# Kernel tuning notes

Measured on AMD Instinct MI355X. Metric: run time of the kernel, lower is better.

## Reference

```python
import jax, jax.numpy as jnp
import numpy as np

# HGT meta: 2 node types (A=0, B=1), 3 relations (src_type, dst_type)
L, T, R = 3, 2, 3
H, D = 1, 64            # PyG HGTConv default heads=1, head_dim = hidden/heads
F = H * D               # hidden_channels = input feature dim = 64
NA = NB = 131072
E = 1_000_000
REL = [(0, 1), (1, 0), (0, 0)]


def setup_inputs() -> dict:
    key = jax.random.key(0)
    ks = jax.random.split(key, 16)
    sc = 1.0 / np.sqrt(F)
    inp = {}
    inp["xA"] = jax.random.normal(ks[0], (NA, F), jnp.float32)
    inp["xB"] = jax.random.normal(ks[1], (NB, F), jnp.float32)
    # K/Q/V projections per (layer, node_type)
    inp["Wk"] = jax.random.normal(ks[2], (L, T, F, F), jnp.float32) * sc
    inp["bk"] = jnp.zeros((L, T, F), jnp.float32)
    inp["Wq"] = jax.random.normal(ks[3], (L, T, F, F), jnp.float32) * sc
    inp["bq"] = jnp.zeros((L, T, F), jnp.float32)
    inp["Wv"] = jax.random.normal(ks[4], (L, T, F, F), jnp.float32) * sc
    inp["bv"] = jnp.zeros((L, T, F), jnp.float32)
    # per (layer, relation, head) attention / message matrices and priority
    inp["a_rel"] = jax.random.normal(ks[5], (L, R, H, D, D), jnp.float32) * sc
    inp["m_rel"] = jax.random.normal(ks[6], (L, R, H, D, D), jnp.float32) * sc
    inp["p_rel"] = jnp.ones((L, R, H), jnp.float32)
    # output projection + skip gate per (layer, node_type)
    inp["Wa"] = jax.random.normal(ks[7], (L, T, F, F), jnp.float32) * sc
    inp["ba"] = jnp.zeros((L, T, F), jnp.float32)
    inp["skip"] = jnp.ones((L, T), jnp.float32)
    # final readout Linear(hidden, 1)
    inp["lin_w"] = jax.random.normal(ks[8], (F, 1), jnp.float32) * sc
    inp["lin_b"] = jnp.zeros((1,), jnp.float32)
    # edge indices: ei[0]=src, ei[1]=dst (NA == NB so one range works)
    inp["ei1"] = jax.random.randint(ks[9], (2, E), 0, NA, jnp.int32)   # A -> B
    inp["ei2"] = jax.random.randint(ks[10], (2, E), 0, NA, jnp.int32)  # B -> A
    inp["ei3"] = jax.random.randint(ks[11], (2, E), 0, NA, jnp.int32)  # A -> A
    return inp


def _hgt_layer(xs, eis, Wk, bk, Wq, bq, Wv, bv, a_rel, m_rel, p_rel, Wa, ba, skip):
    # per-type K/Q/V projections, reshaped to [N, H, D]
    k = [(xs[t] @ Wk[t] + bk[t]).reshape(-1, H, D) for t in range(T)]
    q = [(xs[t] @ Wq[t] + bq[t]).reshape(-1, H, D) for t in range(T)]
    v = [(xs[t] @ Wv[t] + bv[t]).reshape(-1, H, D) for t in range(T)]
    agg = [jnp.zeros((xs[t].shape[0], H, D), xs[t].dtype) for t in range(T)]
    inv_sqrt_d = jnp.asarray(1.0 / np.sqrt(D), xs[0].dtype)
    for r, (s, d) in enumerate(REL):
        src, dst = eis[r][0], eis[r][1]
        n_d = xs[d].shape[0]
        # relation-specific transforms on source nodes, then edge gather
        k_r = jnp.einsum('nhd,hde->nhe', k[s], a_rel[r])
        v_r = jnp.einsum('nhd,hde->nhe', v[s], m_rel[r])
        # attention score per edge per head: (q_dst . k_src) * p_rel / sqrt(D)
        score = jnp.einsum('ehd,ehd->eh', q[d][dst], k_r[src]) * p_rel[r] * inv_sqrt_d
        # segment softmax over incoming edges of each dst node (per edge type)
        mx = jax.ops.segment_max(score, dst, num_segments=n_d)
        ex = jnp.exp(score - mx[dst])
        den = jax.ops.segment_sum(ex, dst, num_segments=n_d)
        alpha = ex / den[dst]                      # [E, H]
        msg = alpha[:, :, None] * v_r[src]         # [E, H, D]
        agg[d] = agg[d] + jax.ops.segment_sum(msg, dst, num_segments=n_d)
    outs = []
    for t in range(T):
        o = jax.nn.gelu(agg[t].reshape(-1, F), approximate=False) @ Wa[t] + ba[t]
        a = jax.nn.sigmoid(skip[t])               # skip gate (out_dim == in_dim)
        outs.append(a * o + (1.0 - a) * xs[t])
    return outs


def reference(xA, xB, Wk, bk, Wq, bq, Wv, bv, a_rel, m_rel, p_rel, Wa, ba, skip,
              lin_w, lin_b, ei1, ei2, ei3):
    xs = [xA, xB]
    eis = [ei1, ei2, ei3]
    for l in range(L):
        xs = _hgt_layer(xs, eis, Wk[l], bk[l], Wq[l], bq[l], Wv[l], bv[l],
                        a_rel[l], m_rel[l], p_rel[l], Wa[l], ba[l], skip[l])
    x = jnp.concatenate(xs, axis=0)               # concat all node types
    pooled = jnp.sum(x, axis=0, keepdims=True)    # global_add_pool, batch=None
    return pooled @ lin_w + lin_b                 # Linear(hidden, 1) -> [1, 1]
```

## Files before the change

kernel.cpp:

```cpp
#include <hip/hip_runtime.h>
#include <cmath>

#define DEV __device__ __forceinline__

typedef __attribute__((ext_vector_type(8))) short short8v;
typedef __attribute__((ext_vector_type(4))) float f32x4;

DEV float atomicAddF(float* p, float v) {
    return unsafeAtomicAdd(p, v);
}

DEV float gelu_exact(float v) {
    return 0.5f * v * (1.f + erff(v * 0.70710678118654752f));
}

DEV unsigned short f32_to_bf16(float f) {
    union { float f; unsigned int u; } x; x.f = f;
    unsigned int r = x.u + 0x7fffu + ((x.u >> 16) & 1u);
    return (unsigned short)(r >> 16);
}

DEV unsigned int f4_to_fp8x4(float a, float b, float c, float d) {
    int r = __builtin_amdgcn_cvt_pk_fp8_f32(a, b, 0, false);
    r = __builtin_amdgcn_cvt_pk_fp8_f32(c, d, r, true);
    return (unsigned int)r;
}

DEV float4 fp8x4_to_f4(unsigned int w) {
    auto lo = __builtin_amdgcn_cvt_pk_f32_fp8(w, false);
    auto hi = __builtin_amdgcn_cvt_pk_f32_fp8(w, true);
    return make_float4(lo[0], lo[1], hi[0], hi[1]);
}

DEV short8v cvt8_bf16(float4 f0, float4 f1) {
    union { unsigned int u[4]; short8v s; } r;
    asm("v_cvt_pk_bf16_f32 %0, %1, %2" : "=v"(r.u[0]) : "v"(f0.x), "v"(f0.y));
    asm("v_cvt_pk_bf16_f32 %0, %1, %2" : "=v"(r.u[1]) : "v"(f0.z), "v"(f0.w));
    asm("v_cvt_pk_bf16_f32 %0, %1, %2" : "=v"(r.u[2]) : "v"(f1.x), "v"(f1.y));
    asm("v_cvt_pk_bf16_f32 %0, %1, %2" : "=v"(r.u[3]) : "v"(f1.z), "v"(f1.w));
    return r.s;
}


struct MatSetB {
    const unsigned short* Wt[3];
    const float* b[3];
    float*       y[3];
    int          mode[3];
    int          n;
};

#define BCAP2 6144
#define SB_TILE 4096
#define PSTR 129

__global__ __launch_bounds__(256) void combine_w_bf16(
    const float* __restrict__ Wk, const float* __restrict__ bk,
    const float* __restrict__ Wv, const float* __restrict__ bv,
    const float* __restrict__ a_rel, const float* __restrict__ m_rel,
    const float* __restrict__ p_rel, unsigned short* __restrict__ CWt,
    float* __restrict__ Cb)
{
    const int r = blockIdx.x, kv = blockIdx.y, l = blockIdx.z;
    const int srcT[3] = {0, 1, 0};
    const int s = srcT[r];
    const float* Wsrc = (kv == 0 ? Wk : Wv) + ((size_t)(l*2 + s)) * 4096;
    const float* bsrc = (kv == 0 ? bk : bv) + ((size_t)(l*2 + s)) * 64;
    const float* A    = (kv == 0 ? a_rel : m_rel) + ((size_t)(l*3 + r)) * 4096;
    const float scale = (kv == 0) ? p_rel[l*3 + r] * 0.125f : 1.f;

    __shared__ float Ws[4096];
    __shared__ float As[4096];
    const int tid = threadIdx.x;
    for (int k = tid; k < 4096; k += 256) { Ws[k] = Wsrc[k]; As[k] = A[k]; }
    __syncthreads();

    unsigned short* out = CWt + ((size_t)(l*6 + r*2 + kv)) * 4096;
    const int j = tid & 63;
    #pragma unroll
    for (int i = 0; i < 16; i++) {
        const int f = (tid >> 6) * 16 + i;
        float acc = 0.f;
        #pragma unroll
        for (int e = 0; e < 64; e++) acc = fmaf(Ws[f*64 + e], As[e*64 + j], acc);
        const int so = (l == 0) ? f : (4*(f & 15) + (f >> 4));
        out[j*64 + so] = f32_to_bf16(acc * scale);
    }
    if (tid < 64) {
        float acc = 0.f;
        for (int e = 0; e < 64; e++) acc = fmaf(bsrc[e], As[e*64 + tid], acc);
        Cb[(size_t)(l*6 + r*2 + kv) * 64 + tid] = acc * scale;
    }
}

__global__ __launch_bounds__(256) void prep_wt(
    const float* __restrict__ Wq, const float* __restrict__ Wa,
    unsigned short* __restrict__ Wqt, unsigned short* __restrict__ Wat)
{
    const int bid = blockIdx.x;
    const float* src; unsigned short* dst; int useSigma;
    if (bid < 6) { src = Wq + (size_t)bid * 4096; dst = Wqt + (size_t)bid * 4096;
                   useSigma = (bid >= 2); }
    else         { src = Wa + (size_t)(bid - 6) * 4096; dst = Wat + (size_t)(bid - 6) * 4096;
                   useSigma = 1; }
    for (int idx = threadIdx.x; idx < 4096; idx += 256) {
        const int c = idx >> 6, s = idx & 63;
        const int k = useSigma ? (16*(s & 3) + (s >> 2)) : s;
        dst[c*64 + s] = f32_to_bf16(src[k*64 + c]);
    }
}

__global__ __launch_bounds__(256) void proj_mfma(const float* __restrict__ x, MatSetB ms)
{
    const int tid = threadIdx.x;
    const int wv  = tid >> 6;
    const int ln  = tid & 63;
    const int j   = ln & 15;
    const int g   = ln >> 4;
    const long long rowb = (long long)blockIdx.x * 128 + wv * 32;

    short8v A[2][2];
    #pragma unroll
    for (int rg = 0; rg < 2; rg++) {
        const float* xp = x + (rowb + rg*16 + j) * 64 + g*8;
        #pragma unroll
        for (int ks = 0; ks < 2; ks++) {
            const float4 f0 = *(const float4*)(xp + ks*32);
            const float4 f1 = *(const float4*)(xp + ks*32 + 4);
            A[rg][ks] = cvt8_bf16(f0, f1);
        }
    }

    unsigned int kst[2][4];
    for (int m = 0; m < ms.n; m++) {
        short8v B[4][2];
        #pragma unroll
        for (int ct = 0; ct < 4; ct++) {
            const unsigned short* wp = ms.Wt[m] + (ct*16 + j) * 64 + g*8;
            B[ct][0] = *(const short8v*)(wp);
            B[ct][1] = *(const short8v*)(wp + 32);
        }
        f32x4 acc[2][4];
        #pragma unroll
        for (int ct = 0; ct < 4; ct++) {
            const float bm = ms.b[m][ct*16 + j];
            f32x4 bi = {bm, bm, bm, bm};
            acc[0][ct] = bi; acc[1][ct] = bi;
        }
        #pragma unroll
        for (int rg = 0; rg < 2; rg++)
            #pragma unroll
            for (int ct = 0; ct < 4; ct++) {
                acc[rg][ct] = __builtin_amdgcn_mfma_f32_16x16x32_bf16(
                    A[rg][0], B[ct][0], acc[rg][ct], 0, 0, 0);
                acc[rg][ct] = __builtin_amdgcn_mfma_f32_16x16x32_bf16(
                    A[rg][1], B[ct][1], acc[rg][ct], 0, 0, 0);
            }
        const int mode = ms.mode[m];
        if (mode == 0) {
            float* yb = ms.y[m];
            #pragma unroll
            for (int rg = 0; rg < 2; rg++)
                #pragma unroll
                for (int i = 0; i < 4; i++) {
                    const long long node = rowb + rg*16 + g*4 + i;
                    *(float4*)(yb + node*64 + j*4) = make_float4(
                        acc[rg][0][i], acc[rg][1][i], acc[rg][2][i], acc[rg][3][i]);
                }
        } else if (mode == 1) {
            #pragma unroll
            for (int rg = 0; rg < 2; rg++)
                #pragma unroll
                for (int i = 0; i < 4; i++)
                    kst[rg][i] = f4_to_fp8x4(
                        acc[rg][0][i], acc[rg][1][i], acc[rg][2][i], acc[rg][3][i]);
        } else {
            unsigned char* yb = (unsigned char*)ms.y[m];
            #pragma unroll
            for (int rg = 0; rg < 2; rg++)
                #pragma unroll
                for (int i = 0; i < 4; i++) {
                    const long long node = rowb + rg*16 + g*4 + i;
                    uint2 s;
                    s.x = kst[rg][i];
                    s.y = f4_to_fp8x4(
                        acc[rg][0][i], acc[rg][1][i], acc[rg][2][i], acc[rg][3][i]);
                    *(uint2*)(yb + node*128 + j*8) = s;
                }
        }
    }
}

__global__ __launch_bounds__(256) void scatter_bucket(
    const int* __restrict__ ei, int E, int nbuck,
    int* __restrict__ bcur, int2* __restrict__ pairbuf)
{
    __shared__ int  hist[256];
    __shared__ int  lbase[256];
    __shared__ int  gbase[256];
    __shared__ int  lcur[256];
    __shared__ int  scanbuf[256];
    __shared__ int2 stage[SB_TILE];
    const int tid = threadIdx.x;
    const int tile0 = blockIdx.x * SB_TILE;

    int2 my[16]; int mb[16];
    #pragma unroll
    for (int i = 0; i < 16; i++) {
        const int e = tile0 + tid + i*256;
        if (e < E) { my[i].x = ei[e]; my[i].y = ei[E + e]; mb[i] = my[i].y >> 9; }
        else mb[i] = -1;
    }
    hist[tid] = 0;
    __syncthreads();
    #pragma unroll
    for (int i = 0; i < 16; i++) if (mb[i] >= 0) atomicAdd(&hist[mb[i]], 1);
    __syncthreads();
    const int c = hist[tid];
    scanbuf[tid] = c;
    __syncthreads();
    for (int off = 1; off < 256; off <<= 1) {
        int add = (tid >= off) ? scanbuf[tid - off] : 0;
        __syncthreads();
        scanbuf[tid] += add;
        __syncthreads();
    }
    lbase[tid] = scanbuf[tid] - c;
    lcur[tid]  = scanbuf[tid] - c;
    if (c > 0 && tid < nbuck) gbase[tid] = atomicAdd(bcur + tid * 16, c);
    __syncthreads();
    #pragma unroll
    for (int i = 0; i < 16; i++) {
        if (mb[i] >= 0) {
            const int p = atomicAdd(&lcur[mb[i]], 1);
            stage[p] = my[i];
        }
    }
    __syncthreads();
    if (c > 0 && tid < nbuck) {
        const int gb = gbase[tid];
        const int lb = lbase[tid];
        int2* dstp = pairbuf + (size_t)tid * BCAP2;
        for (int jj = 0; jj < c; jj++) {
            const int gp = gb + jj;
            if (gp < BCAP2) dstp[gp] = stage[lb + jj];
        }
    }
}

__global__ __launch_bounds__(256) void bucket_csr(
    const int2* __restrict__ pairbuf, const int* __restrict__ bcur,
    int* __restrict__ row_ptr, int* __restrict__ row_end,
    int* __restrict__ col, int n)
{
    const int b   = blockIdx.x;
    const int tid = threadIdx.x;
    __shared__ int lcnt[512];
    __shared__ int lcur[512];
    __shared__ int scanbuf[256];
    int cnt = bcur[b * 16];
    if (cnt > BCAP2) cnt = BCAP2;
    lcnt[tid] = 0; lcnt[tid + 256] = 0;
    __syncthreads();
    const int2* src = pairbuf + (size_t)b * BCAP2;
    for (int i = tid; i < cnt; i += 256)
        atomicAdd(&lcnt[src[i].y & 511], 1);
    __syncthreads();
    const int c0 = lcnt[2*tid], c1 = lcnt[2*tid + 1];
    const int s = c0 + c1;
    scanbuf[tid] = s;
    __syncthreads();
    for (int off = 1; off < 256; off <<= 1) {
        int add = (tid >= off) ? scanbuf[tid - off] : 0;
        __syncthreads();
        scanbuf[tid] += add;
        __syncthreads();
    }
    const int excl = scanbuf[tid] - s;
    const int base = b * BCAP2;
    const int d0 = (b << 9) + 2*tid;
    if (d0 < n)     { row_ptr[d0]   = base + excl;      row_end[d0]   = base + excl + c0; }
    if (d0 + 1 < n) { row_ptr[d0+1] = base + excl + c0; row_end[d0+1] = base + excl + c0 + c1; }
    lcur[2*tid] = excl; lcur[2*tid + 1] = excl + c0;
    __syncthreads();
    for (int i = tid; i < cnt; i += 256) {
        const int2 p = src[i];
        const int pos = atomicAdd(&lcur[p.y & 511], 1);
        col[base + pos] = p.x;
    }
}

__global__ __launch_bounds__(128) void tile_perm(
    const int* __restrict__ rp1, const int* __restrict__ re1,
    const int* __restrict__ rp2, const int* __restrict__ re2,
    int dual, int n, unsigned char* __restrict__ perm)
{
    const int t   = threadIdx.x;
    const int dst = blockIdx.x * 128 + t;
    int deg = 0;
    if (dst < n) {
        deg = re1[dst] - rp1[dst];
        if (dual) deg += re2[dst] - rp2[dst];
    }
    __shared__ int degs[128];
    degs[t] = deg;
    __syncthreads();
    int rank = 0;
    for (int i = 0; i < 128; i++) {
        const int di = degs[i];
        rank += (di > deg) || (di == deg && i < t);
    }
    perm[(size_t)blockIdx.x * 128 + rank] = (unsigned char)t;
}

#define PROC_EDGE(KVR)                                                                 \
    {                                                                                  \
        const float4 ka_ = fp8x4_to_f4(KVR.x);                                         \
        const float4 kb2_ = fp8x4_to_f4(KVR.z);                                        \
        float sc_ = q0.x*ka_.x + q0.y*ka_.y + q0.z*ka_.z + q0.w*ka_.w                  \
                  + q1.x*kb2_.x + q1.y*kb2_.y + q1.z*kb2_.z + q1.w*kb2_.w;             \
        sc_ += __shfl_xor(sc_, 1); sc_ += __shfl_xor(sc_, 2); sc_ += __shfl_xor(sc_, 4);\
        const float p_ = __expf(sc_);                                                  \
        const float4 va_ = fp8x4_to_f4(KVR.y);                                         \
        const float4 vb_ = fp8x4_to_f4(KVR.w);                                         \
        ssum_ += p_;                                                                   \
        acc0_.x = fmaf(p_, va_.x, acc0_.x); acc0_.y = fmaf(p_, va_.y, acc0_.y);        \
        acc0_.z = fmaf(p_, va_.z, acc0_.z); acc0_.w = fmaf(p_, va_.w, acc0_.w);        \
        acc1_.x = fmaf(p_, vb_.x, acc1_.x); acc1_.y = fmaf(p_, vb_.y, acc1_.y);        \
        acc1_.z = fmaf(p_, vb_.z, acc1_.z); acc1_.w = fmaf(p_, vb_.w, acc1_.w);        \
    }

#define AGG_BODY(RP, RE, COL, KV, O0, O1)                                              \
    {                                                                                  \
        float4 acc0_ = {0.f,0.f,0.f,0.f}, acc1_ = {0.f,0.f,0.f,0.f};                   \
        float ssum_ = 0.f;                                                             \
        const int ss0_ = (RP)[dst], ss1_ = (RE)[dst];                                  \
        const unsigned char* kb_ = (KV) + sub*16;                                      \
        int e_ = ss0_;                                                                 \
        uint4 cc0_ = {0,0,0,0}, cc1_ = {0,0,0,0};                                      \
        if (e_ < ss1_)     cc0_ = *(const uint4*)(kb_ + (size_t)(COL)[e_] * 128);      \
        if (e_ + 1 < ss1_) cc1_ = *(const uint4*)(kb_ + (size_t)(COL)[e_+1] * 128);    \
        for (; e_ + 2 < ss1_; e_ += 2) {                                               \
            const int nn0_ = (COL)[e_+2];                                              \
            const int nn1_ = (e_ + 3 < ss1_) ? (COL)[e_+3] : nn0_;                     \
            const uint4 pp0_ = *(const uint4*)(kb_ + (size_t)nn0_ * 128);              \
            const uint4 pp1_ = *(const uint4*)(kb_ + (size_t)nn1_ * 128);              \
            PROC_EDGE(cc0_)                                                            \
            PROC_EDGE(cc1_)                                                            \
            cc0_ = pp0_; cc1_ = pp1_;                                                  \
        }                                                                              \
        if (e_ < ss1_)     PROC_EDGE(cc0_)                                             \
        if (e_ + 1 < ss1_) PROC_EDGE(cc1_)                                             \
        const float inv_ = (ssum_ > 0.f) ? 1.f / ssum_ : 0.f;                          \
        O0.x = fmaf(acc0_.x, inv_, O0.x); O0.y = fmaf(acc0_.y, inv_, O0.y);            \
        O0.z = fmaf(acc0_.z, inv_, O0.z); O0.w = fmaf(acc0_.w, inv_, O0.w);            \
        O1.x = fmaf(acc1_.x, inv_, O1.x); O1.y = fmaf(acc1_.y, inv_, O1.y);            \
        O1.z = fmaf(acc1_.z, inv_, O1.z); O1.w = fmaf(acc1_.w, inv_, O1.w);            \
    }

__global__ __launch_bounds__(1024, 8) void agg_epilogue(
    const int* __restrict__ rp1, const int* __restrict__ re1, const int* __restrict__ c1,
    const int* __restrict__ rp2, const int* __restrict__ re2, const int* __restrict__ c2,
    const float* __restrict__ q,
    const unsigned char* __restrict__ kva, const unsigned char* __restrict__ kvb,
    const unsigned char* __restrict__ perm,
    float* __restrict__ xio, const unsigned short* __restrict__ Wat,
    const float* __restrict__ ba, const float* __restrict__ skipw,
    int xstd, int dual, int dopool, float* __restrict__ vec)
{
    __shared__ float lds[64 * PSTR];
    __shared__ float lds_pool[64];
    const int tid = threadIdx.x;
    const long long rowb = (long long)blockIdx.x * 128;
    if (tid < 64) lds_pool[tid] = 0.f;

    {
        const int sub = tid & 7;
        const int dl  = perm[(size_t)blockIdx.x * 128 + (tid >> 3)];
        const int dst = (int)rowb + dl;
        const float4* qp = (const float4*)(q + (size_t)dst * 64);
        const float4 q0 = qp[sub*2], q1 = qp[sub*2 + 1];
        float4 o0 = {0.f,0.f,0.f,0.f}, o1 = {0.f,0.f,0.f,0.f};
        AGG_BODY(rp1, re1, c1, kva, o0, o1)
        if (dual) {
            AGG_BODY(rp2, re2, c2, kvb, o0, o1)
        }
        float* lp = lds + (size_t)(8*sub) * PSTR + dl;
        lp[0*PSTR] = gelu_exact(o0.x); lp[1*PSTR] = gelu_exact(o0.y);
        lp[2*PSTR] = gelu_exact(o0.z); lp[3*PSTR] = gelu_exact(o0.w);
        lp[4*PSTR] = gelu_exact(o1.x); lp[5*PSTR] = gelu_exact(o1.y);
        lp[6*PSTR] = gelu_exact(o1.z); lp[7*PSTR] = gelu_exact(o1.w);
    }
    __syncthreads();

    if (tid < 512) {
        const int wv = tid >> 6;
        const int ln = tid & 63;
        const int j  = ln & 15;
        const int g  = ln >> 4;
        const int r  = wv*16 + j;

        short8v A[2];
        #pragma unroll
        for (int ks = 0; ks < 2; ks++) {
            const int pb = g*8 + ks*32;
            const float4 f0 = make_float4(lds[(pb+0)*PSTR + r], lds[(pb+1)*PSTR + r],
                                          lds[(pb+2)*PSTR + r], lds[(pb+3)*PSTR + r]);
            const float4 f1 = make_float4(lds[(pb+4)*PSTR + r], lds[(pb+5)*PSTR + r],
                                          lds[(pb+6)*PSTR + r], lds[(pb+7)*PSTR + r]);
            A[ks] = cvt8_bf16(f0, f1);
        }

        f32x4 acc[4];
        #pragma unroll
        for (int ct = 0; ct < 4; ct++) {
            const float bm = ba[ct*16 + j];
            acc[ct] = (f32x4){bm, bm, bm, bm};
        }
        #pragma unroll
        for (int ct = 0; ct < 4; ct++) {
            const unsigned short* wp = Wat + (ct*16 + j) * 64 + g*8;
            const short8v B0 = *(const short8v*)(wp);
            const short8v B1 = *(const short8v*)(wp + 32);
            acc[ct] = __builtin_amdgcn_mfma_f32_16x16x32_bf16(A[0], B0, acc[ct], 0, 0, 0);
            acc[ct] = __builtin_amdgcn_mfma_f32_16x16x32_bf16(A[1], B1, acc[ct], 0, 0, 0);
        }

        const float gate = 1.f / (1.f + __expf(-skipw[0]));
        const float og   = 1.f - gate;
        float4 pacc = {0.f,0.f,0.f,0.f};
        #pragma unroll
        for (int i = 0; i < 4; i++) {
            const long long node = rowb + wv*16 + g*4 + i;
            float* xp = xio + node*64;
            float4 o;
            if (xstd) {
                o.x = gate*acc[0][i] + og*xp[j];
                o.y = gate*acc[1][i] + og*xp[16 + j];
                o.z = gate*acc[2][i] + og*xp[32 + j];
                o.w = gate*acc[3][i] + og*xp[48 + j];
            } else {
                const float4 xo = *(const float4*)(xp + 4*j);
                o = make_float4(gate*acc[0][i] + og*xo.x,
                                gate*acc[1][i] + og*xo.y,
                                gate*acc[2][i] + og*xo.z,
                                gate*acc[3][i] + og*xo.w);
            }
            if (!dopool) {
                *(float4*)(xp + 4*j) = o;
            } else {
                pacc.x += o.x; pacc.y += o.y; pacc.z += o.z; pacc.w += o.w;
            }
        }
        if (dopool) {
            atomicAdd(&lds_pool[4*j + 0], pacc.x);
            atomicAdd(&lds_pool[4*j + 1], pacc.y);
            atomicAdd(&lds_pool[4*j + 2], pacc.z);
            atomicAdd(&lds_pool[4*j + 3], pacc.w);
        }
    }
    __syncthreads();
    if (dopool && tid < 64) atomicAddF(vec + tid, lds_pool[tid]);
}

__global__ void final_dot(const float* __restrict__ vec, const float* __restrict__ lw,
                          const float* __restrict__ lb, float* __restrict__ out)
{
    const int i = threadIdx.x;
    float v = vec[i] * lw[16*(i & 3) + (i >> 2)];
    #pragma unroll
    for (int m = 32; m >= 1; m >>= 1) v += __shfl_xor(v, m);
    if (i == 0) out[0] = v + lb[0];
}

extern "C" void kernel_launch(void* const* d_in, const int* in_sizes, int n_in,
                              void* d_out, int out_size, void* d_ws, size_t ws_size,
                              hipStream_t stream)
{
    float* xs[2] = {(float*)d_in[0], (float*)d_in[1]};
    const float* Wk    = (const float*)d_in[2];
    const float* bk    = (const float*)d_in[3];
    const float* Wq    = (const float*)d_in[4];
    const float* bq    = (const float*)d_in[5];
    const float* Wv    = (const float*)d_in[6];
    const float* bv    = (const float*)d_in[7];
    const float* a_rel = (const float*)d_in[8];
    const float* m_rel = (const float*)d_in[9];
    const float* p_rel = (const float*)d_in[10];
    const float* Wa    = (const float*)d_in[11];
    const float* ba    = (const float*)d_in[12];
    const float* skipw = (const float*)d_in[13];
    const float* lin_w = (const float*)d_in[14];
    const float* lin_b = (const float*)d_in[15];
    const int*   ei[3] = {(const int*)d_in[16], (const int*)d_in[17], (const int*)d_in[18]};

    const long long NA = in_sizes[0] / 64;
    const long long NB = in_sizes[1] / 64;
    const long long Ns[2] = {NA, NB};
    const long long Nmax = NA > NB ? NA : NB;
    int E[3];
    for (int r = 0; r < 3; r++) E[r] = in_sizes[16 + r] / 2;
    static const int dstN_is_B[3] = {1, 0, 0};
    const long long nbuckMax = (Nmax + 511) >> 9;

    float* w = (float*)d_ws;
    float* qbuf  = w; w += Nmax * 64;
    unsigned char* kv0 = (unsigned char*)w; w += Nmax * 32;
    unsigned char* kv1 = (unsigned char*)w; w += Nmax * 32;
    unsigned short* CWt = (unsigned short*)w; w += 18 * 2048;
    unsigned short* Wqt = (unsigned short*)w; w += 6 * 2048;
    unsigned short* Wat = (unsigned short*)w; w += 6 * 2048;
    float* Cb    = w; w += 18 * 64;
    float* vec   = w; w += 64;
    unsigned char* permB = (unsigned char*)w; w += Nmax / 4;
    unsigned char* permA = (unsigned char*)w; w += Nmax / 4;
    int* iw = (int*)w;
    int* row_ptr[3]; int* row_end[3]; int* col[3];
    for (int r = 0; r < 3; r++) {
        row_ptr[r] = iw; iw += Nmax;
        row_end[r] = iw; iw += Nmax;
        col[r]     = iw; iw += nbuckMax * BCAP2;
    }
    int*  bcur    = iw; iw += nbuckMax * 16;
    int2* pairbuf = (int2*)iw;

    combine_w_bf16<<<dim3(3, 2, 3), 256, 0, stream>>>(Wk, bk, Wv, bv, a_rel, m_rel, p_rel, CWt, Cb);
    prep_wt<<<12, 256, 0, stream>>>(Wq, Wa, Wqt, Wat);
    hipMemsetAsync(vec, 0, 64 * sizeof(float), stream);

    for (int r = 0; r < 3; r++) {
        const int n = (int)Ns[dstN_is_B[r]];
        const int nbuck = (n + 511) >> 9;
        hipMemsetAsync(bcur, 0, (size_t)nbuck * 16 * sizeof(int), stream);
        scatter_bucket<<<(E[r] + SB_TILE - 1) / SB_TILE, 256, 0, stream>>>(
            ei[r], E[r], nbuck, bcur, pairbuf);
        bucket_csr<<<nbuck, 256, 0, stream>>>(pairbuf, bcur, row_ptr[r], row_end[r], col[r], n);
    }
    tile_perm<<<(int)((NB + 127) / 128), 128, 0, stream>>>(
        row_ptr[0], row_end[0], row_ptr[0], row_end[0], 0, (int)NB, permB);
    tile_perm<<<(int)((NA + 127) / 128), 128, 0, stream>>>(
        row_ptr[1], row_end[1], row_ptr[2], row_end[2], 1, (int)NA, permA);

    const int gA = (int)(NA >> 7), gB = (int)(NB >> 7);
    for (int l = 0; l < 3; l++) {
        const int xstd   = (l == 0) ? 1 : 0;
        const int dopool = (l == 2) ? 1 : 0;
        {
            MatSetB ms; ms.n = 3;
            ms.Wt[0] = Wqt + (size_t)(l*2 + 1) * 4096;  ms.b[0] = bq + (size_t)(l*2 + 1) * 64;
            ms.y[0] = qbuf;        ms.mode[0] = 0;
            ms.Wt[1] = CWt + (size_t)(l*6 + 2) * 4096;  ms.b[1] = Cb + (size_t)(l*6 + 2) * 64;
            ms.y[1] = nullptr;     ms.mode[1] = 1;
            ms.Wt[2] = CWt + (size_t)(l*6 + 3) * 4096;  ms.b[2] = Cb + (size_t)(l*6 + 3) * 64;
            ms.y[2] = (float*)kv1; ms.mode[2] = 2;
            proj_mfma<<<gB, 256, 0, stream>>>(xs[1], ms);
        }
        {
            MatSetB ms; ms.n = 2;
            ms.Wt[0] = CWt + (size_t)(l*6 + 0) * 4096;  ms.b[0] = Cb + (size_t)(l*6 + 0) * 64;
            ms.y[0] = nullptr;     ms.mode[0] = 1;
            ms.Wt[1] = CWt + (size_t)(l*6 + 1) * 4096;  ms.b[1] = Cb + (size_t)(l*6 + 1) * 64;
            ms.y[1] = (float*)kv0; ms.mode[1] = 2;
            ms.Wt[2] = ms.Wt[1]; ms.b[2] = ms.b[1]; ms.y[2] = ms.y[1]; ms.mode[2] = 2;
            proj_mfma<<<gA, 256, 0, stream>>>(xs[0], ms);
        }
        agg_epilogue<<<gB, 1024, 0, stream>>>(
            row_ptr[0], row_end[0], col[0],
            row_ptr[0], row_end[0], col[0],
            qbuf, kv0, kv0, permB, xs[1],
            Wat + (size_t)(l*2 + 1) * 4096, ba + (size_t)(l*2 + 1) * 64,
            skipw + l*2 + 1, xstd, 0, dopool, vec);

        {
            MatSetB ms; ms.n = 3;
            ms.Wt[0] = Wqt + (size_t)(l*2 + 0) * 4096;  ms.b[0] = bq + (size_t)(l*2 + 0) * 64;
            ms.y[0] = qbuf;        ms.mode[0] = 0;
            ms.Wt[1] = CWt + (size_t)(l*6 + 4) * 4096;  ms.b[1] = Cb + (size_t)(l*6 + 4) * 64;
            ms.y[1] = nullptr;     ms.mode[1] = 1;
            ms.Wt[2] = CWt + (size_t)(l*6 + 5) * 4096;  ms.b[2] = Cb + (size_t)(l*6 + 5) * 64;
            ms.y[2] = (float*)kv0; ms.mode[2] = 2;
            proj_mfma<<<gA, 256, 0, stream>>>(xs[0], ms);
        }
        agg_epilogue<<<gA, 1024, 0, stream>>>(
            row_ptr[1], row_end[1], col[1],
            row_ptr[2], row_end[2], col[2],
            qbuf, kv1, kv0, permA, xs[0],
            Wat + (size_t)(l*2 + 0) * 4096, ba + (size_t)(l*2 + 0) * 64,
            skipw + l*2 + 0, xstd, 1, dopool, vec);
    }

    final_dot<<<1, 64, 0, stream>>>(vec, lin_w, lin_b, (float*)d_out);
}
```

Before: 857.5 us.

## Merge projection launches, co-schedule A-side projection with B aggregation, drop degree permutation

```diff
diff --git a/kernel.cpp b/kernel.cpp
--- a/kernel.cpp
+++ b/kernel.cpp
@@ -110,14 +110,13 @@
     }
 }
 
-__global__ __launch_bounds__(256) void proj_mfma(const float* __restrict__ x, MatSetB ms)
-{
-    const int tid = threadIdx.x;
+DEV void proj128_body(const float* __restrict__ x, const MatSetB& ms, int bid, int tid)
+{
     const int wv  = tid >> 6;
     const int ln  = tid & 63;
     const int j   = ln & 15;
     const int g   = ln >> 4;
-    const long long rowb = (long long)blockIdx.x * 128 + wv * 32;
+    const long long rowb = (long long)bid * 128 + wv * 32;
 
     short8v A[2][2];
     #pragma unroll
@@ -191,6 +190,77 @@
     }
 }
 
+__global__ __launch_bounds__(256) void proj_pair(
+    const float* __restrict__ x1, MatSetB ms1, int g1,
+    const float* __restrict__ x2, MatSetB ms2)
+{
+    const int tid = threadIdx.x;
+    if ((int)blockIdx.x < g1) proj128_body(x1, ms1, blockIdx.x, tid);
+    else                      proj128_body(x2, ms2, blockIdx.x - g1, tid);
+}
+
+DEV void proj16_lean(const float* __restrict__ x, const MatSetB& ms, int bid, int tid)
+{
+    const int wv = tid >> 6;
+    const int ln = tid & 63;
+    const int j  = ln & 15;
+    const int g  = ln >> 4;
+    const long long rowb = (long long)bid * 256 + wv * 16;
+
+    short8v A[2];
+    {
+        const float* xp = x + (rowb + j) * 64 + g*8;
+        #pragma unroll
+        for (int ks = 0; ks < 2; ks++) {
+            const float4 f0 = *(const float4*)(xp + ks*32);
+            const float4 f1 = *(const float4*)(xp + ks*32 + 4);
+            A[ks] = cvt8_bf16(f0, f1);
+        }
+    }
+
+    unsigned int kst[4];
+    for (int m = 0; m < ms.n; m++) {
+        f32x4 acc[4];
+        #pragma unroll
+        for (int ct = 0; ct < 4; ct++) {
+            const float bm = ms.b[m][ct*16 + j];
+            acc[ct] = (f32x4){bm, bm, bm, bm};
+        }
+        #pragma unroll
+        for (int ct = 0; ct < 4; ct++) {
+            const unsigned short* wp = ms.Wt[m] + (ct*16 + j) * 64 + g*8;
+            const short8v B0 = *(const short8v*)(wp);
+            const short8v B1 = *(const short8v*)(wp + 32);
+            acc[ct] = __builtin_amdgcn_mfma_f32_16x16x32_bf16(A[0], B0, acc[ct], 0, 0, 0);
+            acc[ct] = __builtin_amdgcn_mfma_f32_16x16x32_bf16(A[1], B1, acc[ct], 0, 0, 0);
+        }
+        const int mode = ms.mode[m];
+        if (mode == 0) {
+            float* yb = ms.y[m];
+            #pragma unroll
+            for (int i = 0; i < 4; i++) {
+                const long long node = rowb + g*4 + i;
+                *(float4*)(yb + node*64 + j*4) = make_float4(
+                    acc[0][i], acc[1][i], acc[2][i], acc[3][i]);
+            }
+        } else if (mode == 1) {
+            #pragma unroll
+            for (int i = 0; i < 4; i++)
+                kst[i] = f4_to_fp8x4(acc[0][i], acc[1][i], acc[2][i], acc[3][i]);
+        } else {
+            unsigned char* yb = (unsigned char*)ms.y[m];
+            #pragma unroll
+            for (int i = 0; i < 4; i++) {
+                const long long node = rowb + g*4 + i;
+                uint2 s;
+                s.x = kst[i];
+                s.y = f4_to_fp8x4(acc[0][i], acc[1][i], acc[2][i], acc[3][i]);
+                *(uint2*)(yb + node*128 + j*8) = s;
+            }
+        }
+    }
+}
+
 __global__ __launch_bounds__(256) void scatter_bucket(
     const int* __restrict__ ei, int E, int nbuck,
     int* __restrict__ bcur, int2* __restrict__ pairbuf)
@@ -288,29 +358,6 @@
         const int pos = atomicAdd(&lcur[p.y & 511], 1);
         col[base + pos] = p.x;
     }
-}
-
-__global__ __launch_bounds__(128) void tile_perm(
-    const int* __restrict__ rp1, const int* __restrict__ re1,
-    const int* __restrict__ rp2, const int* __restrict__ re2,
-    int dual, int n, unsigned char* __restrict__ perm)
-{
-    const int t   = threadIdx.x;
-    const int dst = blockIdx.x * 128 + t;
-    int deg = 0;
-    if (dst < n) {
-        deg = re1[dst] - rp1[dst];
-        if (dual) deg += re2[dst] - rp2[dst];
-    }
-    __shared__ int degs[128];
-    degs[t] = deg;
-    __syncthreads();
-    int rank = 0;
-    for (int i = 0; i < 128; i++) {
-        const int di = degs[i];
-        rank += (di > deg) || (di == deg && i < t);
-    }
-    perm[(size_t)blockIdx.x * 128 + rank] = (unsigned char)t;
 }
 
 #define PROC_EDGE(KVR)                                                                 \
@@ -358,25 +405,22 @@
         O1.z = fmaf(acc1_.z, inv_, O1.z); O1.w = fmaf(acc1_.w, inv_, O1.w);            \
     }
 
-__global__ __launch_bounds__(1024, 8) void agg_epilogue(
+DEV void agg_block(
     const int* __restrict__ rp1, const int* __restrict__ re1, const int* __restrict__ c1,
     const int* __restrict__ rp2, const int* __restrict__ re2, const int* __restrict__ c2,
     const float* __restrict__ q,
     const unsigned char* __restrict__ kva, const unsigned char* __restrict__ kvb,
-    const unsigned char* __restrict__ perm,
     float* __restrict__ xio, const unsigned short* __restrict__ Wat,
     const float* __restrict__ ba, const float* __restrict__ skipw,
-    int xstd, int dual, int dopool, float* __restrict__ vec)
-{
-    __shared__ float lds[64 * PSTR];
-    __shared__ float lds_pool[64];
-    const int tid = threadIdx.x;
-    const long long rowb = (long long)blockIdx.x * 128;
+    int xstd, int dual, int dopool, float* __restrict__ vec,
+    int bid, int tid, float* lds, float* lds_pool)
+{
+    const long long rowb = (long long)bid * 128;
     if (tid < 64) lds_pool[tid] = 0.f;
 
     {
         const int sub = tid & 7;
-        const int dl  = perm[(size_t)blockIdx.x * 128 + (tid >> 3)];
+        const int dl  = tid >> 3;
         const int dst = (int)rowb + dl;
         const float4* qp = (const float4*)(q + (size_t)dst * 64);
         const float4 q0 = qp[sub*2], q1 = qp[sub*2 + 1];
@@ -463,6 +507,49 @@
     if (dopool && tid < 64) atomicAddF(vec + tid, lds_pool[tid]);
 }
 
+__global__ __launch_bounds__(1024, 8) void agg_epilogue(
+    const int* __restrict__ rp1, const int* __restrict__ re1, const int* __restrict__ c1,
+    const int* __restrict__ rp2, const int* __restrict__ re2, const int* __restrict__ c2,
+    const float* __restrict__ q,
+    const unsigned char* __restrict__ kva, const unsigned char* __restrict__ kvb,
+    float* __restrict__ xio, const unsigned short* __restrict__ Wat,
+    const float* __restrict__ ba, const float* __restrict__ skipw,
+    int xstd, int dual, int dopool, float* __restrict__ vec)
+{
+    __shared__ float lds[64 * PSTR];
+    __shared__ float lds_pool[64];
+    agg_block(rp1, re1, c1, rp2, re2, c2, q, kva, kvb, xio, Wat, ba, skipw,
+              xstd, dual, dopool, vec, blockIdx.x, threadIdx.x, lds, lds_pool);
+}
+
+__global__ __launch_bounds__(1024, 8) void fused_agg_proj(
+    const int* __restrict__ rp, const int* __restrict__ re, const int* __restrict__ colA,
+    const float* __restrict__ q, const unsigned char* __restrict__ kv,
+    float* __restrict__ xio, const unsigned short* __restrict__ Wat,
+    const float* __restrict__ ba, const float* __restrict__ skipw,
+    int xstd, int dopool, float* __restrict__ vec, int aggGrid, int projGrid,
+    const float* __restrict__ xsrc, MatSetB ms)
+{
+    __shared__ float lds[64 * PSTR];
+    __shared__ float lds_pool[64];
+    const int idx = blockIdx.x;
+    const int tid = threadIdx.x;
+    int isProj, bid;
+    if (aggGrid == 2*projGrid) {
+        if (idx % 3 == 2) { isProj = 1; bid = idx / 3; }
+        else              { isProj = 0; bid = idx - (idx + 1) / 3; }
+    } else {
+        isProj = (idx >= aggGrid);
+        bid = isProj ? idx - aggGrid : idx;
+    }
+    if (isProj) {
+        proj16_lean(xsrc, ms, bid, tid);
+    } else {
+        agg_block(rp, re, colA, rp, re, colA, q, kv, kv, xio, Wat, ba, skipw,
+                  xstd, 0, dopool, vec, bid, tid, lds, lds_pool);
+    }
+}
+
 __global__ void final_dot(const float* __restrict__ vec, const float* __restrict__ lw,
                           const float* __restrict__ lb, float* __restrict__ out)
 {
@@ -504,16 +591,16 @@
     const long long nbuckMax = (Nmax + 511) >> 9;
 
     float* w = (float*)d_ws;
-    float* qbuf  = w; w += Nmax * 64;
+    float* qB  = w; w += Nmax * 64;
+    float* qA  = w; w += Nmax * 64;
     unsigned char* kv0 = (unsigned char*)w; w += Nmax * 32;
     unsigned char* kv1 = (unsigned char*)w; w += Nmax * 32;
+    unsigned char* kv2 = (unsigned char*)w; w += Nmax * 32;
     unsigned short* CWt = (unsigned short*)w; w += 18 * 2048;
     unsigned short* Wqt = (unsigned short*)w; w += 6 * 2048;
     unsigned short* Wat = (unsigned short*)w; w += 6 * 2048;
     float* Cb    = w; w += 18 * 64;
     float* vec   = w; w += 64;
-    unsigned char* permB = (unsigned char*)w; w += Nmax / 4;
-    unsigned char* permA = (unsigned char*)w; w += Nmax / 4;
     int* iw = (int*)w;
     int* row_ptr[3]; int* row_end[3]; int* col[3];
     for (int r = 0; r < 3; r++) {
@@ -536,55 +623,47 @@
             ei[r], E[r], nbuck, bcur, pairbuf);
         bucket_csr<<<nbuck, 256, 0, stream>>>(pairbuf, bcur, row_ptr[r], row_end[r], col[r], n);
     }
-    tile_perm<<<(int)((NB + 127) / 128), 128, 0, stream>>>(
-        row_ptr[0], row_end[0], row_ptr[0], row_end[0], 0, (int)NB, permB);
-    tile_perm<<<(int)((NA + 127) / 128), 128, 0, stream>>>(
-        row_ptr[1], row_end[1], row_ptr[2], row_end[2], 1, (int)NA, permA);
 
     const int gA = (int)(NA >> 7), gB = (int)(NB >> 7);
+    const int aggB = (int)(NB >> 7);
+    const int aggA = (int)(NA >> 7);
+    const int prA  = (int)(NA >> 8);
     for (int l = 0; l < 3; l++) {
         const int xstd   = (l == 0) ? 1 : 0;
         const int dopool = (l == 2) ? 1 : 0;
         {
-            MatSetB ms; ms.n = 3;
-            ms.Wt[0] = Wqt + (size_t)(l*2 + 1) * 4096;  ms.b[0] = bq + (size_t)(l*2 + 1) * 64;
-            ms.y[0] = qbuf;        ms.mode[0] = 0;
-            ms.Wt[1] = CWt + (size_t)(l*6 + 2) * 4096;  ms.b[1] = Cb + (size_t)(l*6 + 2) * 64;
-            ms.y[1] = nullptr;     ms.mode[1] = 1;
-            ms.Wt[2] = CWt + (size_t)(l*6 + 3) * 4096;  ms.b[2] = Cb + (size_t)(l*6 + 3) * 64;
-            ms.y[2] = (float*)kv1; ms.mode[2] = 2;
-            proj_mfma<<<gB, 256, 0, stream>>>(xs[1], ms);
+            MatSetB msB; msB.n = 3;
+            msB.Wt[0] = Wqt + (size_t)(l*2 + 1) * 4096;  msB.b[0] = bq + (size_t)(l*2 + 1) * 64;
+            msB.y[0] = qB;         msB.mode[0] = 0;
+            msB.Wt[1] = CWt + (size_t)(l*6 + 2) * 4096;  msB.b[1] = Cb + (size_t)(l*6 + 2) * 64;
+            msB.y[1] = nullptr;    msB.mode[1] = 1;
+            msB.Wt[2] = CWt + (size_t)(l*6 + 3) * 4096;  msB.b[2] = Cb + (size_t)(l*6 + 3) * 64;
+            msB.y[2] = (float*)kv1; msB.mode[2] = 2;
+            MatSetB msA; msA.n = 2;
+            msA.Wt[0] = CWt + (size_t)(l*6 + 0) * 4096;  msA.b[0] = Cb + (size_t)(l*6 + 0) * 64;
+            msA.y[0] = nullptr;    msA.mode[0] = 1;
+            msA.Wt[1] = CWt + (size_t)(l*6 + 1) * 4096;  msA.b[1] = Cb + (size_t)(l*6 + 1) * 64;
+            msA.y[1] = (float*)kv0; msA.mode[1] = 2;
+            msA.Wt[2] = msA.Wt[1]; msA.b[2] = msA.b[1]; msA.y[2] = msA.y[1]; msA.mode[2] = 2;
+            proj_pair<<<gB + gA, 256, 0, stream>>>(xs[1], msB, gB, xs[0], msA);
         }
         {
-            MatSetB ms; ms.n = 2;
-            ms.Wt[0] = CWt + (size_t)(l*6 + 0) * 4096;  ms.b[0] = Cb + (size_t)(l*6 + 0) * 64;
-            ms.y[0] = nullptr;     ms.mode[0] = 1;
-            ms.Wt[1] = CWt + (size_t)(l*6 + 1) * 4096;  ms.b[1] = Cb + (size_t)(l*6 + 1) * 64;
-            ms.y[1] = (float*)kv0; ms.mode[1] = 2;
-            ms.Wt[2] = ms.Wt[1]; ms.b[2] = ms.b[1]; ms.y[2] = ms.y[1]; ms.mode[2] = 2;
-            proj_mfma<<<gA, 256, 0, stream>>>(xs[0], ms);
-        }
-        agg_epilogue<<<gB, 1024, 0, stream>>>(
-            row_ptr[0], row_end[0], col[0],
-            row_ptr[0], row_end[0], col[0],
-            qbuf, kv0, kv0, permB, xs[1],
-            Wat + (size_t)(l*2 + 1) * 4096, ba + (size_t)(l*2 + 1) * 64,
-            skipw + l*2 + 1, xstd, 0, dopool, vec);
-
-        {
-            MatSetB ms; ms.n = 3;
-            ms.Wt[0] = Wqt + (size_t)(l*2 + 0) * 4096;  ms.b[0] = bq + (size_t)(l*2 + 0) * 64;
-            ms.y[0] = qbuf;        ms.mode[0] = 0;
-            ms.Wt[1] = CWt + (size_t)(l*6 + 4) * 4096;  ms.b[1] = Cb + (size_t)(l*6 + 4) * 64;
-            ms.y[1] = nullptr;     ms.mode[1] = 1;
-            ms.Wt[2] = CWt + (size_t)(l*6 + 5) * 4096;  ms.b[2] = Cb + (size_t)(l*6 + 5) * 64;
-            ms.y[2] = (float*)kv0; ms.mode[2] = 2;
-            proj_mfma<<<gA, 256, 0, stream>>>(xs[0], ms);
-        }
-        agg_epilogue<<<gA, 1024, 0, stream>>>(
+            MatSetB ms2; ms2.n = 3;
+            ms2.Wt[0] = Wqt + (size_t)(l*2 + 0) * 4096;  ms2.b[0] = bq + (size_t)(l*2 + 0) * 64;
+            ms2.y[0] = qA;         ms2.mode[0] = 0;
+            ms2.Wt[1] = CWt + (size_t)(l*6 + 4) * 4096;  ms2.b[1] = Cb + (size_t)(l*6 + 4) * 64;
+            ms2.y[1] = nullptr;    ms2.mode[1] = 1;
+            ms2.Wt[2] = CWt + (size_t)(l*6 + 5) * 4096;  ms2.b[2] = Cb + (size_t)(l*6 + 5) * 64;
+            ms2.y[2] = (float*)kv2; ms2.mode[2] = 2;
+            fused_agg_proj<<<aggB + prA, 1024, 0, stream>>>(
+                row_ptr[0], row_end[0], col[0], qB, kv0, xs[1],
+                Wat + (size_t)(l*2 + 1) * 4096, ba + (size_t)(l*2 + 1) * 64,
+                skipw + l*2 + 1, xstd, dopool, vec, aggB, prA, xs[0], ms2);
+        }
+        agg_epilogue<<<aggA, 1024, 0, stream>>>(
             row_ptr[1], row_end[1], col[1],
             row_ptr[2], row_end[2], col[2],
-            qbuf, kv1, kv0, permA, xs[0],
+            qA, kv1, kv2, xs[0],
             Wat + (size_t)(l*2 + 0) * 4096, ba + (size_t)(l*2 + 0) * 64,
             skipw + l*2 + 0, xstd, 1, dopool, vec);
     }
```

After: 817.9 us. 1.05x faster.
